# Kernel optimization log

Measured on AMD Instinct MI355X. Metric: run time of the kernel, lower is better.

Reference implementation:

```python
import jax, jax.numpy as jnp
import numpy as np

N_HEADS = 16
N_KV_HEADS = 4
HEAD_DIM = 128
NEG_INF = -1e9


def setup_inputs() -> dict:
    key = jax.random.key(0)
    ks = jax.random.split(key, 6)
    bs, seq, d_model = 2, 2048, 2048
    x = jax.random.normal(ks[0], (bs, seq, d_model), jnp.float32)
    # RoPE table: theta = 10000^{-2i/head_dim}, angle = pos * theta
    inv_freq = 1.0 / (10000.0 ** (jnp.arange(0, HEAD_DIM, 2, dtype=jnp.float32) / HEAD_DIM))
    ang = jnp.arange(seq, dtype=jnp.float32)[:, None] * inv_freq[None, :]  # [seq, head_dim/2]
    freqs_cos = jnp.cos(ang)
    freqs_sin = jnp.sin(ang)
    # causal additive mask
    mask = jnp.where(jnp.tril(jnp.ones((seq, seq), dtype=bool)), 0.0, NEG_INF).astype(jnp.float32)
    s = 1.0 / np.sqrt(d_model)
    wq = jax.random.normal(ks[1], (d_model, N_HEADS * HEAD_DIM), jnp.float32) * s
    wk = jax.random.normal(ks[2], (d_model, N_KV_HEADS * HEAD_DIM), jnp.float32) * s
    wv = jax.random.normal(ks[3], (d_model, N_KV_HEADS * HEAD_DIM), jnp.float32) * s
    wo = jax.random.normal(ks[4], (N_HEADS * HEAD_DIM, d_model), jnp.float32) * s
    return {"x": x, "freqs_cos": freqs_cos, "freqs_sin": freqs_sin, "mask": mask,
            "wq": wq, "wk": wk, "wv": wv, "wo": wo}


def _rope(t, cos, sin):
    # t: [b, h, s, d]; cos/sin: [s, d/2]
    b, h, s, d = t.shape
    tp = t.reshape(b, h, s, d // 2, 2)
    x0, x1 = tp[..., 0], tp[..., 1]
    c = cos[None, None, :, :]
    sn = sin[None, None, :, :]
    o0 = x0 * c - x1 * sn
    o1 = x0 * sn + x1 * c
    return jnp.stack([o0, o1], axis=-1).reshape(b, h, s, d)


def reference(x, freqs_cos, freqs_sin, mask, wq, wk, wv, wo):
    bs, seq, d_model = x.shape
    rep = N_HEADS // N_KV_HEADS
    q = (x @ wq).reshape(bs, seq, N_HEADS, HEAD_DIM).transpose(0, 2, 1, 3)
    k = (x @ wk).reshape(bs, seq, N_KV_HEADS, HEAD_DIM).transpose(0, 2, 1, 3)
    v = (x @ wv).reshape(bs, seq, N_KV_HEADS, HEAD_DIM).transpose(0, 2, 1, 3)
    q = _rope(q, freqs_cos, freqs_sin)
    k = _rope(k, freqs_cos, freqs_sin)
    # GQA: group q heads over kv heads instead of materially repeating kv
    qg = q.reshape(bs, N_KV_HEADS, rep, seq, HEAD_DIM)
    scores = jnp.einsum('bgrsd,bgtd->bgrst', qg, k) / np.sqrt(HEAD_DIM)
    scores = scores + mask[None, None, None, :, :]
    attn = jax.nn.softmax(scores, axis=-1)
    out = jnp.einsum('bgrst,bgtd->bgrsd', attn, v)
    out = out.reshape(bs, N_HEADS, seq, HEAD_DIM).transpose(0, 2, 1, 3).reshape(bs, seq, -1)
    return out @ wo
```

## Files before the change

kernel.cpp:

```cpp
#include <hip/hip_runtime.h>
#include <hip/hip_bf16.h>

#define SEQ 2048
#define DM 2048
#define NH 16
#define NKV 4
#define HD 128

typedef float f32x4 __attribute__((ext_vector_type(4)));
typedef short s16x8 __attribute__((ext_vector_type(8)));
typedef short s16x4 __attribute__((ext_vector_type(4)));

__device__ inline __hip_bfloat16 f2b(float f) { return __float2bfloat16(f); }
__device__ inline float b2f_us(unsigned short u) { return __uint_as_float(((unsigned)u) << 16); }
__device__ inline short f2b_s(float f) {
    __hip_bfloat16 h = __float2bfloat16(f);
    return *(short*)&h;
}

__global__ void cast_kernel(const float* __restrict__ in, __hip_bfloat16* __restrict__ out, int n) {
    int i = (blockIdx.x * 256 + threadIdx.x) * 4;
    if (i < n) {
        float4 v = *(const float4*)(in + i);
        __hip_bfloat16 o4[4] = {f2b(v.x), f2b(v.y), f2b(v.z), f2b(v.w)};
        *(ushort4*)(out + i) = *(ushort4*)o4;
    }
}

__global__ void transpose_cast(const float* __restrict__ in, __hip_bfloat16* __restrict__ out,
                               int K, int N) {
    __shared__ float tile[32][33];
    int n0 = blockIdx.x * 32, k0 = blockIdx.y * 32;
    int tx = threadIdx.x, ty = threadIdx.y;
    for (int r = ty; r < 32; r += 8)
        tile[r][tx] = in[(size_t)(k0 + r) * N + n0 + tx];
    __syncthreads();
    for (int r = ty; r < 32; r += 8)
        out[(size_t)(n0 + r) * K + k0 + tx] = f2b(tile[tx][r]);
}

template <int OUT_F32>
__global__ __launch_bounds__(256, 2) void gemm_bt(
    const __hip_bfloat16* __restrict__ A,
    const __hip_bfloat16* __restrict__ Bt,
    void* __restrict__ Cp, int M, int N, int Kd) {
    __shared__ __hip_bfloat16 As[128][72];
    __shared__ __hip_bfloat16 Bs[128][72];
    const int m0 = blockIdx.y * 128, n0 = blockIdx.x * 128;
    const int t = threadIdx.x;
    const int wv = t >> 6, lane = t & 63;
    const int wm = (wv >> 1) * 64, wn = (wv & 1) * 64;
    const int lrow = lane & 15, quad = lane >> 4;
    f32x4 acc[4][4];
    f32x4 z4 = {0.f, 0.f, 0.f, 0.f};
    for (int i = 0; i < 4; ++i)
        for (int j = 0; j < 4; ++j) acc[i][j] = z4;

    s16x8 ar[4], br[4];
    auto load_tile = [&](int k0) {
        for (int i = 0; i < 4; ++i) {
            int flat = (i * 256 + t) * 8;
            int row = flat >> 6, col = flat & 63;
            ar[i] = *(const s16x8*)(A + (size_t)(m0 + row) * Kd + k0 + col);
            br[i] = *(const s16x8*)(Bt + (size_t)(n0 + row) * Kd + k0 + col);
        }
    };
    auto store_tile = [&]() {
        for (int i = 0; i < 4; ++i) {
            int flat = (i * 256 + t) * 8;
            int row = flat >> 6, col = flat & 63;
            *(s16x8*)&As[row][col] = ar[i];
            *(s16x8*)&Bs[row][col] = br[i];
        }
    };

    load_tile(0);
    store_tile();
    __syncthreads();

    for (int k0 = 0; k0 < Kd; k0 += 64) {
        bool more = (k0 + 64) < Kd;
        if (more) load_tile(k0 + 64);
        s16x8 af[2][4], bf[2][4];
        for (int kk = 0; kk < 2; ++kk)
            for (int i = 0; i < 4; ++i) {
                af[kk][i] = *(const s16x8*)&As[wm + i * 16 + lrow][kk * 32 + quad * 8];
                bf[kk][i] = *(const s16x8*)&Bs[wn + i * 16 + lrow][kk * 32 + quad * 8];
            }
        for (int kk = 0; kk < 2; ++kk)
            for (int i = 0; i < 4; ++i)
                for (int j = 0; j < 4; ++j)
                    acc[i][j] = __builtin_amdgcn_mfma_f32_16x16x32_bf16(af[kk][i], bf[kk][j],
                                                                        acc[i][j], 0, 0, 0);
        __syncthreads();
        if (more) {
            store_tile();
            __syncthreads();
        }
    }
    for (int i = 0; i < 4; ++i)
        for (int j = 0; j < 4; ++j)
            for (int r = 0; r < 4; ++r) {
                int m = m0 + wm + i * 16 + quad * 4 + r;
                int n = n0 + wn + j * 16 + lrow;
                if (OUT_F32)
                    ((float*)Cp)[(size_t)m * N + n] = acc[i][j][r];
                else
                    ((__hip_bfloat16*)Cp)[(size_t)m * N + n] = f2b(acc[i][j][r]);
            }
}

__global__ void rope_reshape(const __hip_bfloat16* __restrict__ qkv,
                             const float* __restrict__ fcos, const float* __restrict__ fsin,
                             __hip_bfloat16* __restrict__ q, __hip_bfloat16* __restrict__ k) {
    int tok = blockIdx.x;
    int b = tok >> 11, s = tok & 2047;
    const __hip_bfloat16* row = qkv + (size_t)tok * 3072;
    for (int it = threadIdx.x; it < 320; it += 256) {
        int col = it * 8;
        s16x8 v = *(const s16x8*)(row + col);
        int p0 = (col & 127) >> 1;
        f32x4 c4 = *(const f32x4*)(fcos + s * 64 + p0);
        f32x4 s4 = *(const f32x4*)(fsin + s * 64 + p0);
        short outv[8];
        for (int p = 0; p < 4; ++p) {
            float x0 = b2f_us((unsigned short)v[2 * p]);
            float x1 = b2f_us((unsigned short)v[2 * p + 1]);
            outv[2 * p] = f2b_s(x0 * c4[p] - x1 * s4[p]);
            outv[2 * p + 1] = f2b_s(x0 * s4[p] + x1 * c4[p]);
        }
        int d = col & 127;
        if (col < 2048) {
            int h = col >> 7;
            *(s16x8*)(q + ((size_t)((b * NH + h) * SEQ + s)) * HD + d) = *(s16x8*)outv;
        } else {
            int h = (col - 2048) >> 7;
            *(s16x8*)(k + ((size_t)((b * NKV + h) * SEQ + s)) * HD + d) = *(s16x8*)outv;
        }
    }
}

__global__ void vtrans(const __hip_bfloat16* __restrict__ qkv, __hip_bfloat16* __restrict__ vt) {
    __shared__ __hip_bfloat16 tile[128][136];
    int s0 = blockIdx.x * 128;
    int bh = blockIdx.y;
    int b = bh >> 2, kvh = bh & 3;
    int t = threadIdx.x;
    for (int i = 0; i < 8; ++i) {
        int flat = (i * 256 + t) * 8;
        int row = flat >> 7, col = flat & 127;
        *(s16x8*)&tile[row][col] =
            *(const s16x8*)(qkv + (size_t)(b * SEQ + s0 + row) * 3072 + 2560 + kvh * 128 + col);
    }
    __syncthreads();
    for (int i = 0; i < 8; ++i) {
        int dd = i * 16 + (t >> 4);
        int ss = (t & 15) * 8;
        __hip_bfloat16 tmp[8];
        for (int j = 0; j < 8; ++j) tmp[j] = tile[ss + j][dd];
        *(s16x8*)(vt + ((size_t)((b * NKV + kvh) * HD + dd)) * SEQ + s0 + ss) = *(s16x8*)tmp;
    }
}

__global__ __launch_bounds__(256, 3) void attn_kernel(
    const __hip_bfloat16* __restrict__ q, const __hip_bfloat16* __restrict__ k,
    const __hip_bfloat16* __restrict__ vt, __hip_bfloat16* __restrict__ o) {
    __shared__ __hip_bfloat16 Ks[64][136];
    __shared__ __hip_bfloat16 Vs[128][72];
    __shared__ __hip_bfloat16 Ps[4][16][72];

    const int bx = (gridDim.x - 1) - blockIdx.x;
    const int bh = blockIdx.y;
    const int b = bh >> 4, h = bh & 15;
    const int kvh = h >> 2;
    const int t = threadIdx.x;
    const int w = t >> 6, lane = t & 63;
    const int lrow = lane & 15, quad = lane >> 4;
    const int q0 = bx * 64;
    const int qrow = q0 + w * 16 + lrow;
    const float scale = 0.08838834764831845f;

    const __hip_bfloat16* qp = q + ((size_t)((b * NH + h) * SEQ + qrow)) * HD;
    s16x8 qf[4];
    for (int ks = 0; ks < 4; ++ks) qf[ks] = *(const s16x8*)(qp + ks * 32 + quad * 8);

    float m_i = -1e30f, l_i = 0.f;
    f32x4 accO[8];
    f32x4 z4 = {0.f, 0.f, 0.f, 0.f};
    for (int d = 0; d < 8; ++d) accO[d] = z4;

    const __hip_bfloat16* kbase = k + ((size_t)(b * NKV + kvh) * SEQ) * HD;
    const __hip_bfloat16* vbase = vt + ((size_t)(b * NKV + kvh) * HD) * SEQ;

    s16x8 kr[4], vr[4];
    auto load_tile = [&](int kt) {
        for (int i = 0; i < 4; ++i) {
            int flat = (i * 256 + t) * 8;
            kr[i] = *(const s16x8*)(kbase + (size_t)(kt * 64 + (flat >> 7)) * HD + (flat & 127));
            vr[i] = *(const s16x8*)(vbase + (size_t)(flat >> 6) * SEQ + kt * 64 + (flat & 63));
        }
    };
    auto store_tile = [&]() {
        for (int i = 0; i < 4; ++i) {
            int flat = (i * 256 + t) * 8;
            *(s16x8*)&Ks[flat >> 7][flat & 127] = kr[i];
            *(s16x8*)&Vs[flat >> 6][flat & 63] = vr[i];
        }
    };

    const int nkt = bx + 1;
    load_tile(0);
    store_tile();
    __syncthreads();

    for (int kt = 0; kt < nkt; ++kt) {
        bool more = (kt + 1) < nkt;
        if (more) load_tile(kt + 1);
        bool last = (kt == bx);

        float sv[4][4];
        for (int nt = 0; nt < 4; ++nt) {
            f32x4 sacc = z4;
            for (int ks = 0; ks < 4; ++ks) {
                s16x8 kf = *(const s16x8*)&Ks[nt * 16 + lrow][ks * 32 + quad * 8];
                sacc = __builtin_amdgcn_mfma_f32_16x16x32_bf16(kf, qf[ks], sacc, 0, 0, 0);
            }
            for (int r = 0; r < 4; ++r) {
                int key = kt * 64 + nt * 16 + quad * 4 + r;
                sv[nt][r] = (last && key > qrow) ? -1e30f : sacc[r] * scale;
            }
        }
        float mt = -1e30f;
        for (int nt = 0; nt < 4; ++nt)
            for (int r = 0; r < 4; ++r) mt = fmaxf(mt, sv[nt][r]);
        mt = fmaxf(mt, __shfl_xor(mt, 16, 64));
        mt = fmaxf(mt, __shfl_xor(mt, 32, 64));
        float mn = fmaxf(m_i, mt);
        float alpha = __expf(m_i - mn);
        m_i = mn;
        float rs = 0.f;
        for (int nt = 0; nt < 4; ++nt) {
            short ph[4];
            for (int r = 0; r < 4; ++r) {
                float p = __expf(sv[nt][r] - mn);
                rs += p;
                ph[r] = f2b_s(p);
            }
            *(s16x4*)&Ps[w][lrow][nt * 16 + quad * 4] = *(s16x4*)ph;
        }
        rs += __shfl_xor(rs, 16, 64);
        rs += __shfl_xor(rs, 32, 64);
        l_i = l_i * alpha + rs;
        for (int d = 0; d < 8; ++d)
            for (int r = 0; r < 4; ++r) accO[d][r] *= alpha;
        s16x8 pf0 = *(const s16x8*)&Ps[w][lrow][quad * 8];
        s16x8 pf1 = *(const s16x8*)&Ps[w][lrow][32 + quad * 8];
        for (int dt = 0; dt < 8; ++dt) {
            s16x8 vf0 = *(const s16x8*)&Vs[dt * 16 + lrow][quad * 8];
            s16x8 vf1 = *(const s16x8*)&Vs[dt * 16 + lrow][32 + quad * 8];
            accO[dt] = __builtin_amdgcn_mfma_f32_16x16x32_bf16(vf0, pf0, accO[dt], 0, 0, 0);
            accO[dt] = __builtin_amdgcn_mfma_f32_16x16x32_bf16(vf1, pf1, accO[dt], 0, 0, 0);
        }

        __syncthreads();
        if (more) {
            store_tile();
            __syncthreads();
        }
    }
    float inv = 1.0f / l_i;
    __hip_bfloat16* op = o + (size_t)(b * SEQ + qrow) * DM + h * HD;
    for (int dt = 0; dt < 8; ++dt) {
        short ov[4];
        for (int r = 0; r < 4; ++r) ov[r] = f2b_s(accO[dt][r] * inv);
        *(s16x4*)(op + dt * 16 + quad * 4) = *(s16x4*)ov;
    }
}

extern "C" void kernel_launch(void* const* d_in, const int* in_sizes, int n_in,
                              void* d_out, int out_size, void* d_ws, size_t ws_size,
                              hipStream_t stream) {
    (void)in_sizes; (void)n_in; (void)out_size; (void)ws_size;
    const float* x  = (const float*)d_in[0];
    const float* fc = (const float*)d_in[1];
    const float* fs = (const float*)d_in[2];
    const float* wq = (const float*)d_in[4];
    const float* wk = (const float*)d_in[5];
    const float* wv = (const float*)d_in[6];
    const float* wo = (const float*)d_in[7];

    __hip_bfloat16* xb    = (__hip_bfloat16*)d_ws;
    __hip_bfloat16* wqkvt = xb + (size_t)8388608;
    __hip_bfloat16* wot   = wqkvt + (size_t)6291456;
    __hip_bfloat16* qkv   = wot + (size_t)4194304;
    __hip_bfloat16* qb    = xb;
    __hip_bfloat16* kb    = wqkvt;
    __hip_bfloat16* vtb   = wqkvt + (size_t)2097152;
    __hip_bfloat16* attno = qkv;

    cast_kernel<<<8192, 256, 0, stream>>>(x, xb, 8388608);
    transpose_cast<<<dim3(64, 64), dim3(32, 8), 0, stream>>>(wq, wqkvt, 2048, 2048);
    transpose_cast<<<dim3(16, 64), dim3(32, 8), 0, stream>>>(wk, wqkvt + (size_t)2048 * 2048, 2048, 512);
    transpose_cast<<<dim3(16, 64), dim3(32, 8), 0, stream>>>(wv, wqkvt + (size_t)2560 * 2048, 2048, 512);
    transpose_cast<<<dim3(64, 64), dim3(32, 8), 0, stream>>>(wo, wot, 2048, 2048);
    gemm_bt<0><<<dim3(24, 32), 256, 0, stream>>>(xb, wqkvt, qkv, 4096, 3072, 2048);
    rope_reshape<<<4096, 256, 0, stream>>>(qkv, fc, fs, qb, kb);
    vtrans<<<dim3(16, 8), 256, 0, stream>>>(qkv, vtb);
    attn_kernel<<<dim3(32, 32), 256, 0, stream>>>(qb, kb, vtb, attno);
    gemm_bt<1><<<dim3(16, 32), 256, 0, stream>>>(attno, wot, d_out, 4096, 2048, 2048);
}
```

Before: 393.2 us.

## Load GEMM tiles directly to LDS with XOR-swizzled layout

Replaces the register-staged global-to-LDS copy in the bf16 GEMM with direct global_load_lds transfers. The padded tile layout becomes an XOR-swizzled unpadded one, and the occupancy hint rises from 2 to 3 blocks per CU. This removes the register staging and the LDS write instructions and frees registers, but it drops the software prefetch of the next tile, so loads no longer overlap the MFMA work within a block. The code relies on each lane writing its LDS slot in the order the builtin's wave-contiguous addressing expects.

```diff
diff --git a/kernel.cpp b/kernel.cpp
--- a/kernel.cpp
+++ b/kernel.cpp
@@ -16,6 +16,11 @@
 __device__ inline short f2b_s(float f) {
     __hip_bfloat16 h = __float2bfloat16(f);
     return *(short*)&h;
+}
+
+__device__ inline void gl_lds16(const void* g, void* l) {
+    __builtin_amdgcn_global_load_lds((const __attribute__((address_space(1))) void*)g,
+                                     (__attribute__((address_space(3))) void*)l, 16, 0, 0);
 }
 
 __global__ void cast_kernel(const float* __restrict__ in, __hip_bfloat16* __restrict__ out, int n) {
@@ -40,12 +45,12 @@
 }
 
 template <int OUT_F32>
-__global__ __launch_bounds__(256, 2) void gemm_bt(
+__global__ __launch_bounds__(256, 3) void gemm_bt(
     const __hip_bfloat16* __restrict__ A,
     const __hip_bfloat16* __restrict__ Bt,
     void* __restrict__ Cp, int M, int N, int Kd) {
-    __shared__ __hip_bfloat16 As[128][72];
-    __shared__ __hip_bfloat16 Bs[128][72];
+    __shared__ __hip_bfloat16 As[128 * 64];
+    __shared__ __hip_bfloat16 Bs[128 * 64];
     const int m0 = blockIdx.y * 128, n0 = blockIdx.x * 128;
     const int t = threadIdx.x;
     const int wv = t >> 6, lane = t & 63;
@@ -56,46 +61,30 @@
     for (int i = 0; i < 4; ++i)
         for (int j = 0; j < 4; ++j) acc[i][j] = z4;
 
-    s16x8 ar[4], br[4];
-    auto load_tile = [&](int k0) {
+    for (int k0 = 0; k0 < Kd; k0 += 64) {
+        __syncthreads();
         for (int i = 0; i < 4; ++i) {
-            int flat = (i * 256 + t) * 8;
-            int row = flat >> 6, col = flat & 63;
-            ar[i] = *(const s16x8*)(A + (size_t)(m0 + row) * Kd + k0 + col);
-            br[i] = *(const s16x8*)(Bt + (size_t)(n0 + row) * Kd + k0 + col);
-        }
-    };
-    auto store_tile = [&]() {
-        for (int i = 0; i < 4; ++i) {
-            int flat = (i * 256 + t) * 8;
-            int row = flat >> 6, col = flat & 63;
-            *(s16x8*)&As[row][col] = ar[i];
-            *(s16x8*)&Bs[row][col] = br[i];
-        }
-    };
-
-    load_tile(0);
-    store_tile();
-    __syncthreads();
-
-    for (int k0 = 0; k0 < Kd; k0 += 64) {
-        bool more = (k0 + 64) < Kd;
-        if (more) load_tile(k0 + 64);
-        s16x8 af[2][4], bf[2][4];
-        for (int kk = 0; kk < 2; ++kk)
+            int flat = i * 256 + t;
+            int row = flat >> 3;
+            int cb = (flat & 7) ^ (row & 7);
+            gl_lds16(A + (size_t)(m0 + row) * Kd + k0 + cb * 8, &As[flat * 8]);
+            gl_lds16(Bt + (size_t)(n0 + row) * Kd + k0 + cb * 8, &Bs[flat * 8]);
+        }
+        __syncthreads();
+        for (int kk = 0; kk < 2; ++kk) {
+            s16x8 af[4], bf[4];
             for (int i = 0; i < 4; ++i) {
-                af[kk][i] = *(const s16x8*)&As[wm + i * 16 + lrow][kk * 32 + quad * 8];
-                bf[kk][i] = *(const s16x8*)&Bs[wn + i * 16 + lrow][kk * 32 + quad * 8];
-            }
-        for (int kk = 0; kk < 2; ++kk)
+                int ra = wm + i * 16 + lrow;
+                int rb = wn + i * 16 + lrow;
+                int pba = ((kk * 4 + quad) ^ (ra & 7)) * 8;
+                int pbb = ((kk * 4 + quad) ^ (rb & 7)) * 8;
+                af[i] = *(const s16x8*)&As[ra * 64 + pba];
+                bf[i] = *(const s16x8*)&Bs[rb * 64 + pbb];
+            }
             for (int i = 0; i < 4; ++i)
                 for (int j = 0; j < 4; ++j)
-                    acc[i][j] = __builtin_amdgcn_mfma_f32_16x16x32_bf16(af[kk][i], bf[kk][j],
+                    acc[i][j] = __builtin_amdgcn_mfma_f32_16x16x32_bf16(af[i], bf[j],
                                                                         acc[i][j], 0, 0, 0);
-        __syncthreads();
-        if (more) {
-            store_tile();
-            __syncthreads();
         }
     }
     for (int i = 0; i < 4; ++i)
```

After: 377.2 us. 1.04x faster.
